# Kernel tuning notes

Measured on AMD Instinct MI355X. Metric: run time of the kernel, lower is better.

The kernel has to match this reference:

```python
import jax, jax.numpy as jnp
import numpy as np

N_NODES = 50000
N_EDGES = 600000
D_IN = 128
D_HID = 128
D_OUT = 64


def setup_inputs() -> dict:
    key = jax.random.key(0)
    ks = jax.random.split(key, 8)
    x = jax.random.normal(ks[0], (N_NODES, D_IN), dtype=jnp.float32)
    edge_index = jax.random.randint(ks[1], (2, N_EDGES), 0, N_NODES, dtype=jnp.int32)
    s = 0.05
    W1l = jax.random.normal(ks[2], (D_HID, D_IN), dtype=jnp.float32) * s
    b1 = jnp.zeros((D_HID,), dtype=jnp.float32)
    W1r = jax.random.normal(ks[3], (D_HID, D_IN), dtype=jnp.float32) * s
    W2l = jax.random.normal(ks[4], (D_OUT, D_HID), dtype=jnp.float32) * s
    b2 = jnp.zeros((D_OUT,), dtype=jnp.float32)
    W2r = jax.random.normal(ks[5], (D_OUT, D_HID), dtype=jnp.float32) * s
    return {"x": x, "edge_index": edge_index, "W1l": W1l, "b1": b1,
            "W1r": W1r, "W2l": W2l, "b2": b2, "W2r": W2r}


def _sage_conv(x, src, dst, Wl, bl, Wr, n_nodes):
    # mean aggregation of source features at destination nodes
    msg_sum = jax.ops.segment_sum(x[src], dst, num_segments=n_nodes)  # [N, D]
    deg = jax.ops.segment_sum(jnp.ones((src.shape[0], 1), x.dtype), dst,
                              num_segments=n_nodes)                   # [N, 1]
    mean = msg_sum / jnp.maximum(deg, 1.0)
    # out = lin_l(mean_neighbors) + lin_r(x_self); bias only on lin_l (PyG default)
    return mean @ Wl.T + bl + x @ Wr.T


def reference(x, edge_index, W1l, b1, W1r, W2l, b2, W2r):
    src, dst = edge_index[0], edge_index[1]
    n = x.shape[0]
    h = jax.nn.relu(_sage_conv(x, src, dst, W1l, b1, W1r, n))
    # dropout p=0.5 is identity in eval mode (training=False)
    return _sage_conv(h, src, dst, W2l, b2, W2r, n)
```

## Files before the change

### kernel.cpp

```cpp
#include <hip/hip_runtime.h>
#include <hip/hip_bf16.h>

typedef __bf16 bf16x8 __attribute__((ext_vector_type(8)));
typedef float f32x4 __attribute__((ext_vector_type(4)));

#define D_FEAT 128
#define MT_STRIDE 136
#define CHUNK 1024

__device__ __forceinline__ float bits_to_f(unsigned int u) {
    union { unsigned int i; float f; } c; c.i = u; return c.f;
}
__device__ __forceinline__ unsigned short f_to_bf16(float f) {
    __hip_bfloat16 h = (__hip_bfloat16)f;
    return *(unsigned short*)&h;
}
__device__ __forceinline__ float ld(const void* p, int is16, size_t i) {
    return is16 ? (float)((const __hip_bfloat16*)p)[i] : ((const float*)p)[i];
}

__global__ void probe_kernel(const void* x, int* flags) {
    if (threadIdx.x < 64) {
        const unsigned short* u = (const unsigned short*)x;
        unsigned short v = u[threadIdx.x * 2];
        int e = (v >> 7) & 0xFF;
        bool plaus = (e >= 100 && e <= 140);
        unsigned long long m = __ballot(plaus);
        if (threadIdx.x == 0) {
            flags[0] = (__popcll(m) >= 48) ? 1 : 0;
            flags[1] = 1;
        }
    }
}

__global__ void prep_kernel(const void* W1l, const void* b1, const void* W1r,
                            const void* W2l, const void* b2, const void* W2r,
                            const int* __restrict__ flags, unsigned short* wout) {
    int i = blockIdx.x * blockDim.x + threadIdx.x;
    if (i >= 49344) return;
    const int is16 = flags[0];
    const void* s; int base;
    if      (i < 16384) { s = W1l; base = 0; }
    else if (i < 32768) { s = W1r; base = 16384; }
    else if (i < 40960) { s = W2l; base = 32768; }
    else if (i < 49152) { s = W2r; base = 40960; }
    else if (i < 49280) { s = b1;  base = 49152; }
    else                { s = b2;  base = 49280; }
    wout[i] = f_to_bf16(ld(s, is16, i - base));
}

__global__ void conv_kernel(const void* x, const int* __restrict__ flags,
                            unsigned short* __restrict__ xb, int n4) {
    int i = blockIdx.x * blockDim.x + threadIdx.x;
    if (i >= n4) return;
    if (flags[0]) {
        ((uint2*)xb)[i] = ((const uint2*)x)[i];
    } else {
        const float4 v = ((const float4*)x)[i];
        union { unsigned short us[4]; uint2 u; } t;
        t.us[0] = f_to_bf16(v.x); t.us[1] = f_to_bf16(v.y);
        t.us[2] = f_to_bf16(v.z); t.us[3] = f_to_bf16(v.w);
        ((uint2*)xb)[i] = t.u;
    }
}

__global__ void zero_rows_kernel(unsigned short* xb, unsigned short* h, int N) {
    int t = threadIdx.x;
    xb[(size_t)N * D_FEAT + t] = 0;
    h[(size_t)N * D_FEAT + t] = 0;
}

__global__ void count_deg_kernel(const int* __restrict__ dst, int* __restrict__ deg, int E) {
    int i = blockIdx.x * blockDim.x + threadIdx.x;
    if (i < E) atomicAdd(&deg[dst[i]], 1);
}

__global__ void scan1_kernel(const int* __restrict__ deg, int* __restrict__ bsum, int n) {
    __shared__ int ws[4];
    const int lane = threadIdx.x & 63, wv = threadIdx.x >> 6;
    int i0 = blockIdx.x * CHUNK + threadIdx.x * 4;
    int s = 0;
    #pragma unroll
    for (int j = 0; j < 4; ++j)
        if (i0 + j < n) { int d = deg[i0 + j]; s += (d + 3) & ~3; }
    #pragma unroll
    for (int d = 1; d < 64; d <<= 1) s += __shfl_xor(s, d, 64);
    if (lane == 0) ws[wv] = s;
    __syncthreads();
    if (threadIdx.x == 0) bsum[blockIdx.x] = ws[0] + ws[1] + ws[2] + ws[3];
}

__global__ void scan2_kernel(int* __restrict__ bsum, int nb, int* __restrict__ off, int n) {
    int lane = threadIdx.x;
    int v = (lane < nb) ? bsum[lane] : 0;
    int sc = v;
    #pragma unroll
    for (int s = 1; s < 64; s <<= 1) {
        int t = __shfl_up(sc, s, 64);
        if (lane >= s) sc += t;
    }
    if (lane == nb - 1) off[n] = sc;
    if (lane < nb) bsum[lane] = sc - v;
}

__global__ void scan3_kernel(const int* __restrict__ deg, const int* __restrict__ bsum,
                             int* __restrict__ off, int* __restrict__ cursor, int n) {
    __shared__ int ws[4];
    const int lane = threadIdx.x & 63, wv = threadIdx.x >> 6;
    int i0 = blockIdx.x * CHUNK + threadIdx.x * 4;
    int v0 = 0, v1 = 0, v2 = 0, v3 = 0;
    if (i0 + 0 < n) v0 = (deg[i0 + 0] + 3) & ~3;
    if (i0 + 1 < n) v1 = (deg[i0 + 1] + 3) & ~3;
    if (i0 + 2 < n) v2 = (deg[i0 + 2] + 3) & ~3;
    if (i0 + 3 < n) v3 = (deg[i0 + 3] + 3) & ~3;
    int tsum = v0 + v1 + v2 + v3;
    int sc = tsum;
    #pragma unroll
    for (int s = 1; s < 64; s <<= 1) {
        int t = __shfl_up(sc, s, 64);
        if (lane >= s) sc += t;
    }
    if (lane == 63) ws[wv] = sc;
    __syncthreads();
    int woff = 0;
    for (int w = 0; w < wv; ++w) woff += ws[w];
    int p = bsum[blockIdx.x] + woff + (sc - tsum);
    if (i0 + 0 < n) { off[i0 + 0] = p; cursor[i0 + 0] = p; p += v0; }
    if (i0 + 1 < n) { off[i0 + 1] = p; cursor[i0 + 1] = p; p += v1; }
    if (i0 + 2 < n) { off[i0 + 2] = p; cursor[i0 + 2] = p; p += v2; }
    if (i0 + 3 < n) { off[i0 + 3] = p; cursor[i0 + 3] = p; p += v3; }
}

__global__ void fill_kernel(const int* __restrict__ src, const int* __restrict__ dst,
                            int* __restrict__ cursor, int* __restrict__ esrc, int E) {
    int i = blockIdx.x * blockDim.x + threadIdx.x;
    if (i < E) {
        int p = atomicAdd(&cursor[dst[i]], 1);
        esrc[p] = src[i];
    }
}

__global__ void fillpad_kernel(const int* __restrict__ off, const int* __restrict__ deg,
                               int* __restrict__ esrc, int N) {
    int g = blockIdx.x * blockDim.x + threadIdx.x;
    if (g >= N) return;
    int s = off[g] + deg[g];
    int e = off[g] + ((deg[g] + 3) & ~3);
    for (int i = s; i < e; ++i) esrc[i] = N;
}

template <int NOUT, bool RELU>
__global__ __launch_bounds__(256)
void fused_layer_kernel(const unsigned short* __restrict__ feat,
                        const int* __restrict__ off, const int* __restrict__ deg,
                        const int* __restrict__ esrc,
                        const unsigned short* __restrict__ Wl,
                        const unsigned short* __restrict__ Wr,
                        const unsigned short* __restrict__ bias,
                        const int* __restrict__ oflag,
                        void* __restrict__ out, int N) {
    __shared__ unsigned short meanT[32][MT_STRIDE];
    const int tid = threadIdx.x;
    const int lane = tid & 63;
    const int wave = tid >> 6;
    const int node0 = blockIdx.x * 32;
    const int o16 = oflag[0];

    const int a_lo = node0 + wave * 8;
    if (a_lo < N) {
        const int a_hi = min(a_lo + 8, N);
        const int nn = a_hi - a_lo;
        int offv = off[min(a_lo + min(lane, 8), N)];
        int degv = deg[min(a_lo + min(lane, 7), N - 1)];
        #define OFFAT(i) __shfl(offv, (i), 64)
        const int e_beg = OFFAT(0);
        const int e_end = OFFAT(nn);
        const int quarter = lane >> 4;
        const int fl = lane & 15;
        float ax[8];
        #pragma unroll
        for (int i = 0; i < 8; ++i) ax[i] = 0.f;
        int g = a_lo;
        int gend = OFFAT(1);

        auto flush = [&](int gg) {
            int td = __shfl(degv, gg - a_lo, 64);
            float inv = 1.f / (float)(td > 0 ? td : 1);
            unsigned int pk[4];
            #pragma unroll
            for (int i = 0; i < 4; ++i) {
                float v0 = ax[2 * i], v1 = ax[2 * i + 1];
                v0 += __shfl_xor(v0, 16, 64); v0 += __shfl_xor(v0, 32, 64);
                v1 += __shfl_xor(v1, 16, 64); v1 += __shfl_xor(v1, 32, 64);
                pk[i] = (unsigned int)f_to_bf16(v0 * inv)
                      | ((unsigned int)f_to_bf16(v1 * inv) << 16);
                ax[2 * i] = 0.f; ax[2 * i + 1] = 0.f;
            }
            if (quarter == 0)
                *(uint4*)&meanT[gg - node0][fl * 8] = make_uint4(pk[0], pk[1], pk[2], pk[3]);
        };

        int cur = (e_beg < e_end) ? esrc[min(e_beg + (lane & 31), e_end - 1)] : 0;
        for (int e = e_beg; e < e_end; e += 32) {
            int nxt = (e + 32 < e_end) ? esrc[min(e + 32 + (lane & 31), e_end - 1)] : 0;
            uint4 r[8];
            #pragma unroll
            for (int k = 0; k < 8; ++k) {
                int sk = __shfl(cur, 4 * k + quarter, 64);
                r[k] = *(const uint4*)(feat + (size_t)sk * D_FEAT + fl * 8);
            }
            #pragma unroll
            for (int k = 0; k < 8; ++k) {
                const int eb = e + 4 * k;
                if (eb < e_end) {
                    while (eb >= gend) {
                        flush(g);
                        ++g;
                        gend = OFFAT(min(g - a_lo + 1, 8));
                    }
                    uint4 u = r[k];
                    ax[0] += bits_to_f(u.x << 16); ax[1] += bits_to_f(u.x & 0xffff0000u);
                    ax[2] += bits_to_f(u.y << 16); ax[3] += bits_to_f(u.y & 0xffff0000u);
                    ax[4] += bits_to_f(u.z << 16); ax[5] += bits_to_f(u.z & 0xffff0000u);
                    ax[6] += bits_to_f(u.w << 16); ax[7] += bits_to_f(u.w & 0xffff0000u);
                }
            }
            cur = nxt;
        }
        while (g < a_hi) {
            flush(g);
            ++g;
            gend = OFFAT(min(g - a_lo + 1, 8));
        }
        #undef OFFAT
    }
    __syncthreads();

    const int rowg = wave >> 1;
    const int colh = wave & 1;
    constexpr int NT = NOUT / 32;
    const int n_lo = node0 + rowg * 16;
    const int lrow = lane & 15;
    const int kg = lane >> 4;
    f32x4 acc[NT];
    #pragma unroll
    for (int t = 0; t < NT; ++t) acc[t] = (f32x4){0.f, 0.f, 0.f, 0.f};

    const int grow = min(n_lo + lrow, N);
    #pragma unroll
    for (int hh = 0; hh < 2; ++hh) {
        const unsigned short* W = hh ? Wr : Wl;
        #pragma unroll
        for (int ks = 0; ks < 4; ++ks) {
            const int k0 = ks * 32 + kg * 8;
            bf16x8 a;
            if (hh == 0) a = *(const bf16x8*)&meanT[rowg * 16 + lrow][k0];
            else         a = *(const bf16x8*)(feat + (size_t)grow * D_FEAT + k0);
            #pragma unroll
            for (int t = 0; t < NT; ++t) {
                int col16 = colh * NT + t;
                bf16x8 b = *(const bf16x8*)(W + (size_t)(col16 * 16 + lrow) * D_FEAT + k0);
                acc[t] = __builtin_amdgcn_mfma_f32_16x16x32_bf16(a, b, acc[t], 0, 0, 0);
            }
        }
    }
    const int orow0 = n_lo + kg * 4;
    #pragma unroll
    for (int t = 0; t < NT; ++t) {
        const int col = (colh * NT + t) * 16 + lrow;
        float bv = bits_to_f((unsigned int)bias[col] << 16);
        #pragma unroll
        for (int r2 = 0; r2 < 4; ++r2) {
            int orow = orow0 + r2;
            if (orow < N) {
                float v = acc[t][r2] + bv;
                if (RELU) v = fmaxf(v, 0.f);
                if (o16) ((__hip_bfloat16*)out)[(size_t)orow * NOUT + col] = (__hip_bfloat16)v;
                else     ((float*)out)[(size_t)orow * NOUT + col] = v;
            }
        }
    }
}

extern "C" void kernel_launch(void* const* d_in, const int* in_sizes, int n_in,
                              void* d_out, int out_size, void* d_ws, size_t ws_size,
                              hipStream_t stream) {
    const void* x   = d_in[0];
    const int* eidx = (const int*)d_in[1];
    const void* W1l = d_in[2];
    const void* b1  = d_in[3];
    const void* W1r = d_in[4];
    const void* W2l = d_in[5];
    const void* b2  = d_in[6];
    const void* W2r = d_in[7];

    const int N = in_sizes[0] / D_FEAT;
    const int E = in_sizes[1] / 2;
    const int* src = eidx;
    const int* dst = eidx + E;

    char* ws = (char*)d_ws;
    size_t o = 0;
    auto alloc = [&](size_t bytes) -> void* {
        void* p = ws + o;
        o += (bytes + 255) & ~(size_t)255;
        return p;
    };
    int* flags  = (int*)alloc(256);
    int* bsum   = (int*)alloc(64 * 4);
    int* deg    = (int*)alloc((size_t)N * 4);
    int* off    = (int*)alloc((size_t)(N + 1) * 4);
    int* cursor = (int*)alloc((size_t)N * 4);
    int* esrc   = (int*)alloc((size_t)(E + 3 * N + 64) * 4);
    unsigned short* wconv = (unsigned short*)alloc(49344 * 2);
    unsigned short* h  = (unsigned short*)alloc((size_t)(N + 1) * D_FEAT * 2);
    unsigned short* xb = (unsigned short*)alloc((size_t)(N + 1) * D_FEAT * 2);
    (void)n_in; (void)out_size; (void)ws_size;

    probe_kernel<<<1, 64, 0, stream>>>(x, flags);
    prep_kernel<<<(49344 + 255) / 256, 256, 0, stream>>>(W1l, b1, W1r, W2l, b2, W2r, flags, wconv);
    hipMemsetAsync(deg, 0, (size_t)N * 4, stream);
    count_deg_kernel<<<(E + 255) / 256, 256, 0, stream>>>(dst, deg, E);
    const int nchunk = (N + CHUNK - 1) / CHUNK;
    scan1_kernel<<<nchunk, 256, 0, stream>>>(deg, bsum, N);
    scan2_kernel<<<1, 64, 0, stream>>>(bsum, nchunk, off, N);
    scan3_kernel<<<nchunk, 256, 0, stream>>>(deg, bsum, off, cursor, N);
    fill_kernel<<<(E + 255) / 256, 256, 0, stream>>>(src, dst, cursor, esrc, E);
    fillpad_kernel<<<(N + 255) / 256, 256, 0, stream>>>(off, deg, esrc, N);

    const int n4 = N * D_FEAT / 4;
    conv_kernel<<<(n4 + 255) / 256, 256, 0, stream>>>(x, flags, xb, n4);
    zero_rows_kernel<<<1, 128, 0, stream>>>(xb, h, N);

    const int nblocks = (N + 31) / 32;
    fused_layer_kernel<128, true><<<nblocks, 256, 0, stream>>>(
        xb, off, deg, esrc,
        wconv + 0, wconv + 16384, wconv + 49152, flags + 1, h, N);
    fused_layer_kernel<64, false><<<nblocks, 256, 0, stream>>>(
        h, off, deg, esrc,
        wconv + 32768, wconv + 40960, wconv + 49280, flags + 0, d_out, N);
}
```

Measured before the change: 249.6 us.

## Transform-then-aggregate: GEMM before neighbor mean, fuse setup kernels

Reorders each SAGE layer so the linear transform runs first (mean(x)W = mean(xW)), then gathers already-projected bf16 rows. In layer 2 this shrinks the gathered rows from 128 to 64 features, which cuts gather traffic. It also merges the probe, weight-prep and degree-count kernels, folds scan2 and the padding fill into scan3, and drops the separate x conversion pass by converting to bf16 inside the GEMM. The cost is extra round trips through global memory for the projected intermediates, plus rounding the projections to bf16 before averaging.

```diff
diff --git a/kernel.cpp b/kernel.cpp
--- a/kernel.cpp
+++ b/kernel.cpp
@@ -5,8 +5,8 @@
 typedef float f32x4 __attribute__((ext_vector_type(4)));
 
 #define D_FEAT 128
-#define MT_STRIDE 136
 #define CHUNK 1024
+#define NW 49344
 
 __device__ __forceinline__ float bits_to_f(unsigned int u) {
     union { unsigned int i; float f; } c; c.i = u; return c.f;
@@ -18,61 +18,33 @@
 __device__ __forceinline__ float ld(const void* p, int is16, size_t i) {
     return is16 ? (float)((const __hip_bfloat16*)p)[i] : ((const float*)p)[i];
 }
-
-__global__ void probe_kernel(const void* x, int* flags) {
-    if (threadIdx.x < 64) {
-        const unsigned short* u = (const unsigned short*)x;
-        unsigned short v = u[threadIdx.x * 2];
-        int e = (v >> 7) & 0xFF;
-        bool plaus = (e >= 100 && e <= 140);
-        unsigned long long m = __ballot(plaus);
-        if (threadIdx.x == 0) {
-            flags[0] = (__popcll(m) >= 48) ? 1 : 0;
-            flags[1] = 1;
-        }
-    }
-}
-
-__global__ void prep_kernel(const void* W1l, const void* b1, const void* W1r,
-                            const void* W2l, const void* b2, const void* W2r,
-                            const int* __restrict__ flags, unsigned short* wout) {
+__device__ __forceinline__ int wave_probe16(const void* p) {
+    const unsigned short v = ((const unsigned short*)p)[(threadIdx.x & 63) * 2];
+    int e = (v >> 7) & 0xFF;
+    unsigned long long m = __ballot(e >= 100 && e <= 140);
+    return (__popcll(m) >= 48) ? 1 : 0;
+}
+
+__global__ void setup_kernel(const void* x,
+                             const void* W1l, const void* b1, const void* W1r,
+                             const void* W2l, const void* b2, const void* W2r,
+                             const int* __restrict__ dst, int E,
+                             unsigned short* __restrict__ wout, int* __restrict__ deg) {
     int i = blockIdx.x * blockDim.x + threadIdx.x;
-    if (i >= 49344) return;
-    const int is16 = flags[0];
-    const void* s; int base;
-    if      (i < 16384) { s = W1l; base = 0; }
-    else if (i < 32768) { s = W1r; base = 16384; }
-    else if (i < 40960) { s = W2l; base = 32768; }
-    else if (i < 49152) { s = W2r; base = 40960; }
-    else if (i < 49280) { s = b1;  base = 49152; }
-    else                { s = b2;  base = 49280; }
-    wout[i] = f_to_bf16(ld(s, is16, i - base));
-}
-
-__global__ void conv_kernel(const void* x, const int* __restrict__ flags,
-                            unsigned short* __restrict__ xb, int n4) {
-    int i = blockIdx.x * blockDim.x + threadIdx.x;
-    if (i >= n4) return;
-    if (flags[0]) {
-        ((uint2*)xb)[i] = ((const uint2*)x)[i];
+    if (i < NW) {
+        int is16 = wave_probe16(x);
+        const void* s; int base;
+        if      (i < 16384) { s = W1l; base = 0; }
+        else if (i < 32768) { s = W1r; base = 16384; }
+        else if (i < 40960) { s = W2l; base = 32768; }
+        else if (i < 49152) { s = W2r; base = 40960; }
+        else if (i < 49280) { s = b1;  base = 49152; }
+        else                { s = b2;  base = 49280; }
+        wout[i] = f_to_bf16(ld(s, is16, i - base));
     } else {
-        const float4 v = ((const float4*)x)[i];
-        union { unsigned short us[4]; uint2 u; } t;
-        t.us[0] = f_to_bf16(v.x); t.us[1] = f_to_bf16(v.y);
-        t.us[2] = f_to_bf16(v.z); t.us[3] = f_to_bf16(v.w);
-        ((uint2*)xb)[i] = t.u;
-    }
-}
-
-__global__ void zero_rows_kernel(unsigned short* xb, unsigned short* h, int N) {
-    int t = threadIdx.x;
-    xb[(size_t)N * D_FEAT + t] = 0;
-    h[(size_t)N * D_FEAT + t] = 0;
-}
-
-__global__ void count_deg_kernel(const int* __restrict__ dst, int* __restrict__ deg, int E) {
-    int i = blockIdx.x * blockDim.x + threadIdx.x;
-    if (i < E) atomicAdd(&deg[dst[i]], 1);
+        int j = i - NW;
+        if (j < E) atomicAdd(&deg[dst[j]], 1);
+    }
 }
 
 __global__ void scan1_kernel(const int* __restrict__ deg, int* __restrict__ bsum, int n) {
@@ -90,29 +62,28 @@
     if (threadIdx.x == 0) bsum[blockIdx.x] = ws[0] + ws[1] + ws[2] + ws[3];
 }
 
-__global__ void scan2_kernel(int* __restrict__ bsum, int nb, int* __restrict__ off, int n) {
-    int lane = threadIdx.x;
-    int v = (lane < nb) ? bsum[lane] : 0;
-    int sc = v;
-    #pragma unroll
-    for (int s = 1; s < 64; s <<= 1) {
-        int t = __shfl_up(sc, s, 64);
-        if (lane >= s) sc += t;
-    }
-    if (lane == nb - 1) off[n] = sc;
-    if (lane < nb) bsum[lane] = sc - v;
-}
-
 __global__ void scan3_kernel(const int* __restrict__ deg, const int* __restrict__ bsum,
-                             int* __restrict__ off, int* __restrict__ cursor, int n) {
+                             int nb, int* __restrict__ off, int* __restrict__ cursor,
+                             int* __restrict__ esrc, int n) {
     __shared__ int ws[4];
     const int lane = threadIdx.x & 63, wv = threadIdx.x >> 6;
+    int bv = (lane < nb) ? bsum[lane] : 0;
+    int bsc = bv;
+    #pragma unroll
+    for (int s = 1; s < 64; s <<= 1) {
+        int t = __shfl_up(bsc, s, 64);
+        if (lane >= s) bsc += t;
+    }
+    const int base = __shfl(bsc, blockIdx.x, 64) - __shfl(bv, blockIdx.x, 64);
+    const int total = __shfl(bsc, nb - 1, 64);
+
     int i0 = blockIdx.x * CHUNK + threadIdx.x * 4;
-    int v0 = 0, v1 = 0, v2 = 0, v3 = 0;
-    if (i0 + 0 < n) v0 = (deg[i0 + 0] + 3) & ~3;
-    if (i0 + 1 < n) v1 = (deg[i0 + 1] + 3) & ~3;
-    if (i0 + 2 < n) v2 = (deg[i0 + 2] + 3) & ~3;
-    if (i0 + 3 < n) v3 = (deg[i0 + 3] + 3) & ~3;
+    int d0 = 0, d1 = 0, d2 = 0, d3 = 0;
+    if (i0 + 0 < n) d0 = deg[i0 + 0];
+    if (i0 + 1 < n) d1 = deg[i0 + 1];
+    if (i0 + 2 < n) d2 = deg[i0 + 2];
+    if (i0 + 3 < n) d3 = deg[i0 + 3];
+    int v0 = (d0 + 3) & ~3, v1 = (d1 + 3) & ~3, v2 = (d2 + 3) & ~3, v3 = (d3 + 3) & ~3;
     int tsum = v0 + v1 + v2 + v3;
     int sc = tsum;
     #pragma unroll
@@ -124,11 +95,16 @@
     __syncthreads();
     int woff = 0;
     for (int w = 0; w < wv; ++w) woff += ws[w];
-    int p = bsum[blockIdx.x] + woff + (sc - tsum);
-    if (i0 + 0 < n) { off[i0 + 0] = p; cursor[i0 + 0] = p; p += v0; }
-    if (i0 + 1 < n) { off[i0 + 1] = p; cursor[i0 + 1] = p; p += v1; }
-    if (i0 + 2 < n) { off[i0 + 2] = p; cursor[i0 + 2] = p; p += v2; }
-    if (i0 + 3 < n) { off[i0 + 3] = p; cursor[i0 + 3] = p; p += v3; }
+    int p = base + woff + (sc - tsum);
+    #define EMIT(idx, dj, vj)                                            \
+        if (i0 + idx < n) {                                              \
+            off[i0 + idx] = p; cursor[i0 + idx] = p;                     \
+            for (int q = p + dj; q < p + vj; ++q) esrc[q] = n;           \
+            p += vj;                                                     \
+        }
+    EMIT(0, d0, v0) EMIT(1, d1, v1) EMIT(2, d2, v2) EMIT(3, d3, v3)
+    #undef EMIT
+    if (blockIdx.x == 0 && threadIdx.x == 0) off[n] = total;
 }
 
 __global__ void fill_kernel(const int* __restrict__ src, const int* __restrict__ dst,
@@ -140,146 +116,232 @@
     }
 }
 
-__global__ void fillpad_kernel(const int* __restrict__ off, const int* __restrict__ deg,
-                               int* __restrict__ esrc, int N) {
-    int g = blockIdx.x * blockDim.x + threadIdx.x;
-    if (g >= N) return;
-    int s = off[g] + deg[g];
-    int e = off[g] + ((deg[g] + 3) & ~3);
-    for (int i = s; i < e; ++i) esrc[i] = N;
-}
-
-template <int NOUT, bool RELU>
+template <int NOUT, bool PROBE_A>
 __global__ __launch_bounds__(256)
-void fused_layer_kernel(const unsigned short* __restrict__ feat,
-                        const int* __restrict__ off, const int* __restrict__ deg,
-                        const int* __restrict__ esrc,
-                        const unsigned short* __restrict__ Wl,
-                        const unsigned short* __restrict__ Wr,
-                        const unsigned short* __restrict__ bias,
-                        const int* __restrict__ oflag,
-                        void* __restrict__ out, int N) {
-    __shared__ unsigned short meanT[32][MT_STRIDE];
-    const int tid = threadIdx.x;
-    const int lane = tid & 63;
-    const int wave = tid >> 6;
-    const int node0 = blockIdx.x * 32;
-    const int o16 = oflag[0];
-
-    const int a_lo = node0 + wave * 8;
-    if (a_lo < N) {
-        const int a_hi = min(a_lo + 8, N);
-        const int nn = a_hi - a_lo;
-        int offv = off[min(a_lo + min(lane, 8), N)];
-        int degv = deg[min(a_lo + min(lane, 7), N - 1)];
-        #define OFFAT(i) __shfl(offv, (i), 64)
-        const int e_beg = OFFAT(0);
-        const int e_end = OFFAT(nn);
-        const int quarter = lane >> 4;
-        const int fl = lane & 15;
-        float ax[8];
-        #pragma unroll
-        for (int i = 0; i < 8; ++i) ax[i] = 0.f;
-        int g = a_lo;
-        int gend = OFFAT(1);
-
-        auto flush = [&](int gg) {
-            int td = __shfl(degv, gg - a_lo, 64);
-            float inv = 1.f / (float)(td > 0 ? td : 1);
+void gemm_dual_kernel(const void* __restrict__ A,
+                      const unsigned short* __restrict__ Wa,
+                      const unsigned short* __restrict__ Wb,
+                      const unsigned short* __restrict__ bias,
+                      unsigned short* __restrict__ za, unsigned short* __restrict__ zb,
+                      unsigned int* __restrict__ zrow, int zrow_words, int N) {
+    if (blockIdx.x == 0 && threadIdx.x < zrow_words) zrow[threadIdx.x] = 0;
+    int a16 = 1;
+    if (PROBE_A) a16 = wave_probe16(A);
+
+    const int lane = threadIdx.x & 63;
+    const int wave = threadIdx.x >> 6;
+    const int m0 = (blockIdx.x * 4 + wave) * 16;
+    if (m0 >= N) return;
+    const int lrow = lane & 15;
+    const int kg = lane >> 4;
+    const int grow = min(m0 + lrow, N - 1);
+    constexpr int NT = NOUT / 16;
+    f32x4 aL[NT], aR[NT];
+    #pragma unroll
+    for (int t = 0; t < NT; ++t) { aL[t] = (f32x4){0,0,0,0}; aR[t] = (f32x4){0,0,0,0}; }
+
+    #pragma unroll
+    for (int ks = 0; ks < 4; ++ks) {
+        const int k0 = ks * 32 + kg * 8;
+        bf16x8 a;
+        if (a16) {
+            a = *(const bf16x8*)((const unsigned short*)A + (size_t)grow * D_FEAT + k0);
+        } else {
+            const float* fp = (const float*)A + (size_t)grow * D_FEAT + k0;
+            float4 f0 = *(const float4*)fp, f1 = *(const float4*)(fp + 4);
+            union { bf16x8 v; unsigned short us[8]; } t;
+            t.us[0] = f_to_bf16(f0.x); t.us[1] = f_to_bf16(f0.y);
+            t.us[2] = f_to_bf16(f0.z); t.us[3] = f_to_bf16(f0.w);
+            t.us[4] = f_to_bf16(f1.x); t.us[5] = f_to_bf16(f1.y);
+            t.us[6] = f_to_bf16(f1.z); t.us[7] = f_to_bf16(f1.w);
+            a = t.v;
+        }
+        #pragma unroll
+        for (int t = 0; t < NT; ++t) {
+            bf16x8 bL = *(const bf16x8*)(Wa + (size_t)(t * 16 + lrow) * D_FEAT + k0);
+            aL[t] = __builtin_amdgcn_mfma_f32_16x16x32_bf16(a, bL, aL[t], 0, 0, 0);
+            bf16x8 bR = *(const bf16x8*)(Wb + (size_t)(t * 16 + lrow) * D_FEAT + k0);
+            aR[t] = __builtin_amdgcn_mfma_f32_16x16x32_bf16(a, bR, aR[t], 0, 0, 0);
+        }
+    }
+    const int orow0 = m0 + kg * 4;
+    #pragma unroll
+    for (int t = 0; t < NT; ++t) {
+        const int col = t * 16 + lrow;
+        float bv = bits_to_f((unsigned int)bias[col] << 16);
+        #pragma unroll
+        for (int r = 0; r < 4; ++r) {
+            int orow = orow0 + r;
+            if (orow < N) {
+                za[(size_t)orow * NOUT + col] = f_to_bf16(aL[t][r]);
+                zb[(size_t)orow * NOUT + col] = f_to_bf16(aR[t][r] + bv);
+            }
+        }
+    }
+}
+
+__global__ __launch_bounds__(256)
+void agg1_kernel(const unsigned short* __restrict__ zl,
+                 unsigned short* __restrict__ h,
+                 const int* __restrict__ off, const int* __restrict__ deg,
+                 const int* __restrict__ esrc, int N) {
+    const int lane = threadIdx.x & 63;
+    const int wave = threadIdx.x >> 6;
+    const int a_lo = (blockIdx.x * 4 + wave) * 8;
+    if (a_lo >= N) return;
+    const int a_hi = min(a_lo + 8, N);
+    const int nn = a_hi - a_lo;
+    int offv = off[min(a_lo + min(lane, 8), N)];
+    int degv = deg[min(a_lo + min(lane, 7), N - 1)];
+    #define OFFAT(i) __shfl(offv, (i), 64)
+    const int e_beg = OFFAT(0);
+    const int e_end = OFFAT(nn);
+    const int quarter = lane >> 4;
+    const int fl = lane & 15;
+    float ax[8];
+    #pragma unroll
+    for (int i = 0; i < 8; ++i) ax[i] = 0.f;
+    int g = a_lo;
+    int gend = OFFAT(1);
+
+    auto flush = [&](int gg) {
+        int td = __shfl(degv, gg - a_lo, 64);
+        float inv = 1.f / (float)(td > 0 ? td : 1);
+        float v[8];
+        #pragma unroll
+        for (int i = 0; i < 8; ++i) {
+            float s = ax[i];
+            s += __shfl_xor(s, 16, 64); s += __shfl_xor(s, 32, 64);
+            v[i] = s * inv; ax[i] = 0.f;
+        }
+        if (quarter == 0) {
+            unsigned short* hp = h + (size_t)gg * D_FEAT + fl * 8;
+            uint4 zr = *(const uint4*)hp;
+            unsigned int w[4] = {zr.x, zr.y, zr.z, zr.w};
             unsigned int pk[4];
             #pragma unroll
             for (int i = 0; i < 4; ++i) {
-                float v0 = ax[2 * i], v1 = ax[2 * i + 1];
-                v0 += __shfl_xor(v0, 16, 64); v0 += __shfl_xor(v0, 32, 64);
-                v1 += __shfl_xor(v1, 16, 64); v1 += __shfl_xor(v1, 32, 64);
-                pk[i] = (unsigned int)f_to_bf16(v0 * inv)
-                      | ((unsigned int)f_to_bf16(v1 * inv) << 16);
-                ax[2 * i] = 0.f; ax[2 * i + 1] = 0.f;
+                float r0 = fmaxf(v[2 * i]     + bits_to_f(w[i] << 16), 0.f);
+                float r1 = fmaxf(v[2 * i + 1] + bits_to_f(w[i] & 0xffff0000u), 0.f);
+                pk[i] = (unsigned int)f_to_bf16(r0) | ((unsigned int)f_to_bf16(r1) << 16);
             }
-            if (quarter == 0)
-                *(uint4*)&meanT[gg - node0][fl * 8] = make_uint4(pk[0], pk[1], pk[2], pk[3]);
-        };
-
-        int cur = (e_beg < e_end) ? esrc[min(e_beg + (lane & 31), e_end - 1)] : 0;
-        for (int e = e_beg; e < e_end; e += 32) {
-            int nxt = (e + 32 < e_end) ? esrc[min(e + 32 + (lane & 31), e_end - 1)] : 0;
-            uint4 r[8];
-            #pragma unroll
-            for (int k = 0; k < 8; ++k) {
-                int sk = __shfl(cur, 4 * k + quarter, 64);
-                r[k] = *(const uint4*)(feat + (size_t)sk * D_FEAT + fl * 8);
+            *(uint4*)hp = make_uint4(pk[0], pk[1], pk[2], pk[3]);
+        }
+    };
+
+    int cur = (e_beg < e_end) ? esrc[min(e_beg + (lane & 31), e_end - 1)] : 0;
+    for (int e = e_beg; e < e_end; e += 32) {
+        int nxt = (e + 32 < e_end) ? esrc[min(e + 32 + (lane & 31), e_end - 1)] : 0;
+        uint4 r[8];
+        #pragma unroll
+        for (int k = 0; k < 8; ++k) {
+            int sk = __shfl(cur, 4 * k + quarter, 64);
+            r[k] = *(const uint4*)(zl + (size_t)sk * D_FEAT + fl * 8);
+        }
+        #pragma unroll
+        for (int k = 0; k < 8; ++k) {
+            const int eb = e + 4 * k;
+            if (eb < e_end) {
+                while (eb >= gend) {
+                    flush(g); ++g;
+                    gend = OFFAT(min(g - a_lo + 1, 8));
+                }
+                uint4 u = r[k];
+                ax[0] += bits_to_f(u.x << 16); ax[1] += bits_to_f(u.x & 0xffff0000u);
+                ax[2] += bits_to_f(u.y << 16); ax[3] += bits_to_f(u.y & 0xffff0000u);
+                ax[4] += bits_to_f(u.z << 16); ax[5] += bits_to_f(u.z & 0xffff0000u);
+                ax[6] += bits_to_f(u.w << 16); ax[7] += bits_to_f(u.w & 0xffff0000u);
             }
-            #pragma unroll
-            for (int k = 0; k < 8; ++k) {
-                const int eb = e + 4 * k;
-                if (eb < e_end) {
-                    while (eb >= gend) {
-                        flush(g);
-                        ++g;
-                        gend = OFFAT(min(g - a_lo + 1, 8));
-                    }
-                    uint4 u = r[k];
-                    ax[0] += bits_to_f(u.x << 16); ax[1] += bits_to_f(u.x & 0xffff0000u);
-                    ax[2] += bits_to_f(u.y << 16); ax[3] += bits_to_f(u.y & 0xffff0000u);
-                    ax[4] += bits_to_f(u.z << 16); ax[5] += bits_to_f(u.z & 0xffff0000u);
-                    ax[6] += bits_to_f(u.w << 16); ax[7] += bits_to_f(u.w & 0xffff0000u);
+        }
+        cur = nxt;
+    }
+    while (g < a_hi) {
+        flush(g); ++g;
+        gend = OFFAT(min(g - a_lo + 1, 8));
+    }
+    #undef OFFAT
+}
+
+__global__ __launch_bounds__(256)
+void agg2_kernel(const unsigned short* __restrict__ z2l,
+                 const unsigned short* __restrict__ s2,
+                 void* __restrict__ out, const void* __restrict__ x,
+                 const int* __restrict__ off, const int* __restrict__ deg,
+                 const int* __restrict__ esrc, int N) {
+    const int o16 = wave_probe16(x);
+    const int lane = threadIdx.x & 63;
+    const int wave = threadIdx.x >> 6;
+    const int a_lo = (blockIdx.x * 4 + wave) * 8;
+    if (a_lo >= N) return;
+    const int a_hi = min(a_lo + 8, N);
+    const int nn = a_hi - a_lo;
+    int offv = off[min(a_lo + min(lane, 8), N)];
+    int degv = deg[min(a_lo + min(lane, 7), N - 1)];
+    #define OFFAT(i) __shfl(offv, (i), 64)
+    const int e_beg = OFFAT(0);
+    const int e_end = OFFAT(nn);
+    const int quarter = lane >> 4;
+    const int fl = lane & 15;
+    float ax[4];
+    #pragma unroll
+    for (int i = 0; i < 4; ++i) ax[i] = 0.f;
+    int g = a_lo;
+    int gend = OFFAT(1);
+
+    auto flush = [&](int gg) {
+        int td = __shfl(degv, gg - a_lo, 64);
+        float inv = 1.f / (float)(td > 0 ? td : 1);
+        float v[4];
+        #pragma unroll
+        for (int i = 0; i < 4; ++i) {
+            float s = ax[i];
+            s += __shfl_xor(s, 16, 64); s += __shfl_xor(s, 32, 64);
+            v[i] = s * inv; ax[i] = 0.f;
+        }
+        if (quarter == 0) {
+            uint2 sb = *(const uint2*)(s2 + (size_t)gg * 64 + fl * 4);
+            v[0] += bits_to_f(sb.x << 16); v[1] += bits_to_f(sb.x & 0xffff0000u);
+            v[2] += bits_to_f(sb.y << 16); v[3] += bits_to_f(sb.y & 0xffff0000u);
+            if (o16) {
+                unsigned int p0 = (unsigned int)f_to_bf16(v[0]) | ((unsigned int)f_to_bf16(v[1]) << 16);
+                unsigned int p1 = (unsigned int)f_to_bf16(v[2]) | ((unsigned int)f_to_bf16(v[3]) << 16);
+                *(uint2*)((unsigned short*)out + (size_t)gg * 64 + fl * 4) = make_uint2(p0, p1);
+            } else {
+                *(float4*)((float*)out + (size_t)gg * 64 + fl * 4) =
+                    make_float4(v[0], v[1], v[2], v[3]);
+            }
+        }
+    };
+
+    int cur = (e_beg < e_end) ? esrc[min(e_beg + (lane & 31), e_end - 1)] : 0;
+    for (int e = e_beg; e < e_end; e += 32) {
+        int nxt = (e + 32 < e_end) ? esrc[min(e + 32 + (lane & 31), e_end - 1)] : 0;
+        uint2 r[8];
+        #pragma unroll
+        for (int k = 0; k < 8; ++k) {
+            int sk = __shfl(cur, 4 * k + quarter, 64);
+            r[k] = *(const uint2*)(z2l + (size_t)sk * 64 + fl * 4);
+        }
+        #pragma unroll
+        for (int k = 0; k < 8; ++k) {
+            const int eb = e + 4 * k;
+            if (eb < e_end) {
+                while (eb >= gend) {
+                    flush(g); ++g;
+                    gend = OFFAT(min(g - a_lo + 1, 8));
                 }
+                uint2 u = r[k];
+                ax[0] += bits_to_f(u.x << 16); ax[1] += bits_to_f(u.x & 0xffff0000u);
+                ax[2] += bits_to_f(u.y << 16); ax[3] += bits_to_f(u.y & 0xffff0000u);
             }
-            cur = nxt;
-        }
-        while (g < a_hi) {
-            flush(g);
-            ++g;
-            gend = OFFAT(min(g - a_lo + 1, 8));
-        }
-        #undef OFFAT
-    }
-    __syncthreads();
-
-    const int rowg = wave >> 1;
-    const int colh = wave & 1;
-    constexpr int NT = NOUT / 32;
-    const int n_lo = node0 + rowg * 16;
-    const int lrow = lane & 15;
-    const int kg = lane >> 4;
-    f32x4 acc[NT];
-    #pragma unroll
-    for (int t = 0; t < NT; ++t) acc[t] = (f32x4){0.f, 0.f, 0.f, 0.f};
-
-    const int grow = min(n_lo + lrow, N);
-    #pragma unroll
-    for (int hh = 0; hh < 2; ++hh) {
-        const unsigned short* W = hh ? Wr : Wl;
-        #pragma unroll
-        for (int ks = 0; ks < 4; ++ks) {
-            const int k0 = ks * 32 + kg * 8;
-            bf16x8 a;
-            if (hh == 0) a = *(const bf16x8*)&meanT[rowg * 16 + lrow][k0];
-            else         a = *(const bf16x8*)(feat + (size_t)grow * D_FEAT + k0);
-            #pragma unroll
-            for (int t = 0; t < NT; ++t) {
-                int col16 = colh * NT + t;
-                bf16x8 b = *(const bf16x8*)(W + (size_t)(col16 * 16 + lrow) * D_FEAT + k0);
-                acc[t] = __builtin_amdgcn_mfma_f32_16x16x32_bf16(a, b, acc[t], 0, 0, 0);
-            }
-        }
-    }
-    const int orow0 = n_lo + kg * 4;
-    #pragma unroll
-    for (int t = 0; t < NT; ++t) {
-        const int col = (colh * NT + t) * 16 + lrow;
-        float bv = bits_to_f((unsigned int)bias[col] << 16);
-        #pragma unroll
-        for (int r2 = 0; r2 < 4; ++r2) {
-            int orow = orow0 + r2;
-            if (orow < N) {
-                float v = acc[t][r2] + bv;
-                if (RELU) v = fmaxf(v, 0.f);
-                if (o16) ((__hip_bfloat16*)out)[(size_t)orow * NOUT + col] = (__hip_bfloat16)v;
-                else     ((float*)out)[(size_t)orow * NOUT + col] = v;
-            }
-        }
-    }
+        }
+        cur = nxt;
+    }
+    while (g < a_hi) {
+        flush(g); ++g;
+        gend = OFFAT(min(g - a_lo + 1, 8));
+    }
+    #undef OFFAT
 }
 
 extern "C" void kernel_launch(void* const* d_in, const int* in_sizes, int n_in,
@@ -306,37 +368,34 @@
         o += (bytes + 255) & ~(size_t)255;
         return p;
     };
-    int* flags  = (int*)alloc(256);
-    int* bsum   = (int*)alloc(64 * 4);
     int* deg    = (int*)alloc((size_t)N * 4);
     int* off    = (int*)alloc((size_t)(N + 1) * 4);
     int* cursor = (int*)alloc((size_t)N * 4);
+    int* bsum   = (int*)alloc(64 * 4);
     int* esrc   = (int*)alloc((size_t)(E + 3 * N + 64) * 4);
-    unsigned short* wconv = (unsigned short*)alloc(49344 * 2);
-    unsigned short* h  = (unsigned short*)alloc((size_t)(N + 1) * D_FEAT * 2);
-    unsigned short* xb = (unsigned short*)alloc((size_t)(N + 1) * D_FEAT * 2);
+    unsigned short* wconv = (unsigned short*)alloc(NW * 2);
+    unsigned short* zl = (unsigned short*)alloc((size_t)(N + 1) * D_FEAT * 2);
+    unsigned short* h  = (unsigned short*)alloc((size_t)N * D_FEAT * 2);
+    unsigned short* z2l = zl;
+    unsigned short* s2  = zl + (size_t)(N + 1) * 64;
     (void)n_in; (void)out_size; (void)ws_size;
 
-    probe_kernel<<<1, 64, 0, stream>>>(x, flags);
-    prep_kernel<<<(49344 + 255) / 256, 256, 0, stream>>>(W1l, b1, W1r, W2l, b2, W2r, flags, wconv);
     hipMemsetAsync(deg, 0, (size_t)N * 4, stream);
-    count_deg_kernel<<<(E + 255) / 256, 256, 0, stream>>>(dst, deg, E);
+    setup_kernel<<<(NW + E + 255) / 256, 256, 0, stream>>>(
+        x, W1l, b1, W1r, W2l, b2, W2r, dst, E, wconv, deg);
     const int nchunk = (N + CHUNK - 1) / CHUNK;
     scan1_kernel<<<nchunk, 256, 0, stream>>>(deg, bsum, N);
-    scan2_kernel<<<1, 64, 0, stream>>>(bsum, nchunk, off, N);
-    scan3_kernel<<<nchunk, 256, 0, stream>>>(deg, bsum, off, cursor, N);
+    scan3_kernel<<<nchunk, 256, 0, stream>>>(deg, bsum, nchunk, off, cursor, esrc, N);
     fill_kernel<<<(E + 255) / 256, 256, 0, stream>>>(src, dst, cursor, esrc, E);
-    fillpad_kernel<<<(N + 255) / 256, 256, 0, stream>>>(off, deg, esrc, N);
-
-    const int n4 = N * D_FEAT / 4;
-    conv_kernel<<<(n4 + 255) / 256, 256, 0, stream>>>(x, flags, xb, n4);
-    zero_rows_kernel<<<1, 128, 0, stream>>>(xb, h, N);
-
-    const int nblocks = (N + 31) / 32;
-    fused_layer_kernel<128, true><<<nblocks, 256, 0, stream>>>(
-        xb, off, deg, esrc,
-        wconv + 0, wconv + 16384, wconv + 49152, flags + 1, h, N);
-    fused_layer_kernel<64, false><<<nblocks, 256, 0, stream>>>(
-        h, off, deg, esrc,
-        wconv + 32768, wconv + 40960, wconv + 49280, flags + 0, d_out, N);
-}
+
+    const int gblocks = (N + 63) / 64;
+    const int ablocks = (N + 31) / 32;
+    gemm_dual_kernel<128, true><<<gblocks, 256, 0, stream>>>(
+        x, wconv + 0, wconv + 16384, wconv + 49152,
+        zl, h, (unsigned int*)(zl + (size_t)N * D_FEAT), 64, N);
+    agg1_kernel<<<ablocks, 256, 0, stream>>>(zl, h, off, deg, esrc, N);
+    gemm_dual_kernel<64, false><<<gblocks, 256, 0, stream>>>(
+        h, wconv + 32768, wconv + 40960, wconv + 49280,
+        z2l, s2, (unsigned int*)(z2l + (size_t)N * 64), 32, N);
+    agg2_kernel<<<ablocks, 256, 0, stream>>>(z2l, s2, d_out, x, off, deg, esrc, N);
+}
```

Result: slower. 257.5 us (+3.2%).
